# Performance work log

Measured on AMD Instinct MI355X. Metric: run time of the kernel, lower is better.

## Reference

```python
import jax, jax.numpy as jnp
import numpy as np

N, M = 32768, 12          # atoms, neighbors
ORIG, NBR, AF, HF = 92, 41, 64, 128
N_CONV = 3
ATOMS_PER = 32            # atoms per crystal
B = N // ATOMS_PER        # number of crystals
EPS = 1e-5                # BatchNorm eps


def softplus(x):
    return jnp.logaddexp(x, 0.0)


def setup_inputs() -> dict:
    key = jax.random.key(0)
    ks = jax.random.split(key, 24)
    s = 0.05
    return {
        "atom_fea": jax.random.normal(ks[0], (N, ORIG), jnp.float32),
        "nbr_fea": jax.random.normal(ks[1], (N, M, NBR), jnp.float32),
        "nbr_fea_idx": jax.random.randint(ks[2], (N, M), 0, N),
        "crystal_id": jnp.arange(N, dtype=jnp.int32) // ATOMS_PER,
        # embedding: Linear(ORIG -> AF)
        "emb_W": jax.random.normal(ks[3], (ORIG, AF), jnp.float32) * s,
        "emb_b": jnp.zeros((AF,), jnp.float32),
        # per-conv-layer params, stacked over N_CONV
        "conv_W": jax.random.normal(ks[4], (N_CONV, 2 * AF + NBR, 2 * AF), jnp.float32) * s,
        "conv_b": jnp.zeros((N_CONV, 2 * AF), jnp.float32),
        "bn1_g": jnp.ones((N_CONV, 2 * AF), jnp.float32),
        "bn1_b": jnp.zeros((N_CONV, 2 * AF), jnp.float32),
        "bn2_g": jnp.ones((N_CONV, AF), jnp.float32),
        "bn2_b": jnp.zeros((N_CONV, AF), jnp.float32),
        # head: conv_to_fc (AF->HF), fcs[0] (HF->HF), fc_out (HF->1)
        "fc1_W": jax.random.normal(ks[5], (AF, HF), jnp.float32) * s,
        "fc1_b": jnp.zeros((HF,), jnp.float32),
        "fc2_W": jax.random.normal(ks[6], (HF, HF), jnp.float32) * s,
        "fc2_b": jnp.zeros((HF,), jnp.float32),
        "out_W": jax.random.normal(ks[7], (HF, 1), jnp.float32) * s,
        "out_b": jnp.zeros((1,), jnp.float32),
    }


def _batchnorm(x, g, b):
    # training-mode BN over the batch (row) axis, biased variance like torch
    mu = x.mean(axis=0)
    var = x.var(axis=0)
    return (x - mu) * jax.lax.rsqrt(var + EPS) * g + b


def reference(atom_fea, nbr_fea, nbr_fea_idx, crystal_id,
              emb_W, emb_b, conv_W, conv_b, bn1_g, bn1_b, bn2_g, bn2_b,
              fc1_W, fc1_b, fc2_W, fc2_b, out_W, out_b):
    x = atom_fea @ emb_W + emb_b                              # (N, AF)
    for l in range(N_CONV):
        nbr_atom = x[nbr_fea_idx]                             # gather (N, M, AF)
        self_fea = jnp.broadcast_to(x[:, None, :], (N, M, AF))
        tot = jnp.concatenate([self_fea, nbr_atom, nbr_fea], axis=2)  # (N,M,2AF+NBR)
        g = tot @ conv_W[l] + conv_b[l]                       # (N, M, 2AF)
        g = _batchnorm(g.reshape(N * M, 2 * AF), bn1_g[l], bn1_b[l]).reshape(N, M, 2 * AF)
        nbr_filter = jax.nn.sigmoid(g[..., :AF])
        nbr_core = softplus(g[..., AF:])
        summed = jnp.sum(nbr_filter * nbr_core, axis=1)       # (N, AF)
        summed = _batchnorm(summed, bn2_g[l], bn2_b[l])
        x = softplus(x + summed)
    # mean pooling per crystal (equal-size crystals of ATOMS_PER atoms)
    pool = jax.ops.segment_sum(x, crystal_id, num_segments=B) / ATOMS_PER  # (B, AF)
    # seq2: softplus -> conv_to_fc -> dropout(p=0) -> softplus -> Linear -> softplus -> dropout(p=0)
    h = softplus(pool)
    h = softplus(h @ fc1_W + fc1_b)
    h = softplus(h @ fc2_W + fc2_b)
    return h @ out_W + out_b                                  # (B, 1)
```

## Files before the change

### kernel.cpp

```cpp
#include <hip/hip_runtime.h>
#include <cmath>

#define DEV __device__ __forceinline__

constexpr int NA    = 32768;
constexpr int M     = 12;
constexpr int ORIG  = 92;
constexpr int NBR   = 41;
constexpr int AF    = 64;
constexpr int C2    = 128;
constexpr int HF    = 128;
constexpr int NCONV = 3;
constexpr int NM    = NA * M;
constexpr int BB    = 1024;
constexpr int TA    = 4;
constexpr int RT    = TA * M;
constexpr int NTILES = NA / TA;
constexpr int GRID_CONV = 2048;
constexpr int GRID_APPLY = 2048;
constexpr int WLD   = 132;
constexpr int ALD   = 44;

DEV float fsig(float x) { return __builtin_amdgcn_rcpf(1.f + __expf(-x)); }
DEV float fsp (float x) { return fmaxf(x, 0.f) + __logf(1.f + __expf(-fabsf(x))); }

DEV void fma4(float4& a, float s, const float4 w) {
    a.x = fmaf(s, w.x, a.x); a.y = fmaf(s, w.y, a.y);
    a.z = fmaf(s, w.z, a.z); a.w = fmaf(s, w.w, a.w);
}
DEV void fma2(float2& a, float s, const float2 w) {
    a.x = fmaf(s, w.x, a.x); a.y = fmaf(s, w.y, a.y);
}
DEV float comp4(const float4 v, int i) { return i == 0 ? v.x : i == 1 ? v.y : i == 2 ? v.z : v.w; }
DEV void add2(float2& a, const float2 b) { a.x += b.x; a.y += b.y; }
DEV void sqa2(float2& a, const float2 b) { a.x = fmaf(b.x, b.x, a.x); a.y = fmaf(b.y, b.y, a.y); }
DEV float2 shxor2(const float2 v, int m) {
    float2 r; r.x = __shfl_xor(v.x, m, 64); r.y = __shfl_xor(v.y, m, 64); return r;
}
DEV unsigned bf16pair(float a, float b) {
    unsigned ua = __float_as_uint(a), ub = __float_as_uint(b);
    ua += 0x7fffu + ((ua >> 16) & 1u);
    ub += 0x7fffu + ((ub >> 16) & 1u);
    return (ua >> 16) | (ub & 0xffff0000u);
}
DEV float2 up2(unsigned u) {
    float2 r;
    r.x = __uint_as_float(u << 16);
    r.y = __uint_as_float(u & 0xffff0000u);
    return r;
}

template<bool FIRST>
__global__ __launch_bounds__(256, 4)
void spx_kernel(const float* __restrict__ xin,
                const float* __restrict__ summed,
                const float* __restrict__ ss2,
                const float* __restrict__ atom_fea,
                const float* __restrict__ embW,
                const float* __restrict__ embb,
                const float* __restrict__ W,
                const float* __restrict__ bias,
                float* __restrict__ xout,
                float* __restrict__ S,
                unsigned* __restrict__ Pb)
{
    __shared__ float xs[16][AF];
    __shared__ float af[FIRST ? 16 * ORIG : 4];

    const int a0 = blockIdx.x * 16, tid = threadIdx.x;

    if (FIRST) {
        for (int i = tid; i < 16 * ORIG; i += 256) af[i] = atom_fea[(size_t)a0 * ORIG + i];
        __syncthreads();
        const int row = tid >> 4, c4 = (tid & 15) * 4;
        float4 acc = *(const float4*)(embb + c4);
        #pragma unroll 4
        for (int k = 0; k < ORIG; ++k)
            fma4(acc, af[row * ORIG + k], *(const float4*)(embW + k * AF + c4));
        *(float4*)&xs[row][c4] = acc;
        *(float4*)(xout + (size_t)(a0 + row) * AF + c4) = acc;
    } else {
        const int row = tid >> 4, c4 = (tid & 15) * 4;
        const size_t o = (size_t)(a0 + row) * AF + c4;
        const float4 xi = *(const float4*)(xin + o);
        const float4 sm = *(const float4*)(summed + o);
        const float4 sc = *(const float4*)(ss2 + c4);
        const float4 sh = *(const float4*)(ss2 + AF + c4);
        float4 ov;
        ov.x = fsp(xi.x + fmaf(sm.x, sc.x, sh.x));
        ov.y = fsp(xi.y + fmaf(sm.y, sc.y, sh.y));
        ov.z = fsp(xi.z + fmaf(sm.z, sc.z, sh.z));
        ov.w = fsp(xi.w + fmaf(sm.w, sc.w, sh.w));
        *(float4*)&xs[row][c4] = ov;
        *(float4*)(xout + o) = ov;
    }
    __syncthreads();

    const int cid = tid & 31, rid = tid >> 5;
    const int c0 = cid * 8, r0 = rid * 2;
    const bool isS = (c0 < 128);
    const int cc = c0 & 127;
    const float* Wb = W + (isS ? 0 : AF * C2) + cc;
    float4 a00, a01, a10, a11;
    if (isS) { a00 = *(const float4*)(bias + cc); a01 = *(const float4*)(bias + cc + 4); }
    else     { a00 = {0,0,0,0}; a01 = {0,0,0,0}; }
    a10 = a00; a11 = a01;
    for (int k = 0; k < AF; ++k) {
        const float4 w0 = *(const float4*)(Wb + k * C2);
        const float4 w1 = *(const float4*)(Wb + k * C2 + 4);
        const float x0 = xs[r0][k], x1 = xs[r0 + 1][k];
        fma4(a00, x0, w0); fma4(a01, x0, w1);
        fma4(a10, x1, w0); fma4(a11, x1, w1);
    }
    if (isS) {
        *(float4*)(S + (size_t)(a0 + r0) * C2 + cc)     = a00;
        *(float4*)(S + (size_t)(a0 + r0) * C2 + cc + 4) = a01;
        *(float4*)(S + (size_t)(a0 + r0 + 1) * C2 + cc)     = a10;
        *(float4*)(S + (size_t)(a0 + r0 + 1) * C2 + cc + 4) = a11;
    } else {
        uint4 u0, u1;
        u0.x = bf16pair(a00.x, a00.y); u0.y = bf16pair(a00.z, a00.w);
        u0.z = bf16pair(a01.x, a01.y); u0.w = bf16pair(a01.z, a01.w);
        u1.x = bf16pair(a10.x, a10.y); u1.y = bf16pair(a10.z, a10.w);
        u1.z = bf16pair(a11.x, a11.y); u1.w = bf16pair(a11.z, a11.w);
        *(uint4*)(Pb + (size_t)(a0 + r0) * 64 + cc / 2)     = u0;
        *(uint4*)(Pb + (size_t)(a0 + r0 + 1) * 64 + cc / 2) = u1;
    }
}

__global__ __launch_bounds__(256, 4)
void conv8_kernel(const float* __restrict__ nbr_fea,
                  const int* __restrict__ idx,
                  const float* __restrict__ W2,
                  const float* __restrict__ S,
                  const unsigned* __restrict__ Pb,
                  float* __restrict__ P1s, float* __restrict__ P1q,
                  unsigned* __restrict__ gout)
{
    __shared__ float W2h[NBR * WLD];
    __shared__ float sA[RT * ALD];

    const int tid  = threadIdx.x;
    const int cid  = tid & 31;
    const int rid  = tid >> 5;
    const int c2   = cid * 2;
    const int r0   = rid * 6;
    const int atom = rid >> 1;

    const int q0 = blockIdx.x;

    int j[6];
    float2 svf, svc;
    float st[8];
    {
        const int n0 = q0 * TA;
        const int ib = n0 * M + r0;
        #pragma unroll
        for (int e = 0; e < 6; ++e) j[e] = idx[ib + e];
        svf = *(const float2*)(S + (size_t)(n0 + atom) * C2 + c2);
        svc = *(const float2*)(S + (size_t)(n0 + atom) * C2 + 64 + c2);
        const float* src = nbr_fea + (size_t)n0 * M * NBR;
        #pragma unroll
        for (int i = 0; i < 8; ++i)
            if (i < 7 || tid + 256 * i < RT * NBR) st[i] = src[tid + 256 * i];
    }

    for (int i = tid; i < NBR * 32; i += 256) {
        const int k = i >> 5, q = i & 31;
        *(float4*)&W2h[k * WLD + q * 4] = *(const float4*)(W2 + k * C2 + q * 4);
    }

    float2 sum_f = {0,0}, sum_c = {0,0}, sq_f = {0,0}, sq_c = {0,0};

    for (int it = 0; it < 4; ++it) {
        const int t  = q0 + it * GRID_CONV;
        const int n0 = t * TA;

        unsigned uf[6], uc[6];
        #pragma unroll
        for (int e = 0; e < 6; ++e) {
            uf[e] = Pb[(size_t)j[e] * 64 + cid];
            uc[e] = Pb[(size_t)j[e] * 64 + 32 + cid];
        }
        const float2 cf = svf, cc = svc;

        __syncthreads();
        #pragma unroll
        for (int i = 0; i < 8; ++i) {
            const int e = tid + 256 * i;
            if (i < 7 || e < RT * NBR) {
                const int r = (int)(((unsigned)e * 102301u) >> 22);
                sA[r * ALD + (e - r * NBR)] = st[i];
            }
        }
        __syncthreads();

        if (it < 3) {
            const int nn0 = (t + GRID_CONV) * TA;
            const int ib = nn0 * M + r0;
            #pragma unroll
            for (int e = 0; e < 6; ++e) j[e] = idx[ib + e];
            svf = *(const float2*)(S + (size_t)(nn0 + atom) * C2 + c2);
            svc = *(const float2*)(S + (size_t)(nn0 + atom) * C2 + 64 + c2);
            const float* src = nbr_fea + (size_t)nn0 * M * NBR;
            #pragma unroll
            for (int i = 0; i < 8; ++i)
                if (i < 7 || tid + 256 * i < RT * NBR) st[i] = src[tid + 256 * i];
        }

        float2 ef0 = {0,0}, ef1 = {0,0}, ef2 = {0,0}, ef3 = {0,0}, ef4 = {0,0}, ef5 = {0,0};
        float2 ec0 = {0,0}, ec1 = {0,0}, ec2 = {0,0}, ec3 = {0,0}, ec4 = {0,0}, ec5 = {0,0};
        const float* Ab = sA + r0 * ALD;
        #pragma unroll 2
        for (int k4 = 0; k4 < 10; ++k4) {
            const float4 a0 = *(const float4*)(Ab + 0 * ALD + k4 * 4);
            const float4 a1 = *(const float4*)(Ab + 1 * ALD + k4 * 4);
            const float4 a2 = *(const float4*)(Ab + 2 * ALD + k4 * 4);
            const float4 a3 = *(const float4*)(Ab + 3 * ALD + k4 * 4);
            const float4 a4 = *(const float4*)(Ab + 4 * ALD + k4 * 4);
            const float4 a5 = *(const float4*)(Ab + 5 * ALD + k4 * 4);
            #pragma unroll
            for (int kk = 0; kk < 4; ++kk) {
                const int k = 4 * k4 + kk;
                const float2 wf = *(const float2*)(W2h + k * WLD + c2);
                const float2 wc = *(const float2*)(W2h + k * WLD + 64 + c2);
                fma2(ef0, comp4(a0, kk), wf); fma2(ec0, comp4(a0, kk), wc);
                fma2(ef1, comp4(a1, kk), wf); fma2(ec1, comp4(a1, kk), wc);
                fma2(ef2, comp4(a2, kk), wf); fma2(ec2, comp4(a2, kk), wc);
                fma2(ef3, comp4(a3, kk), wf); fma2(ec3, comp4(a3, kk), wc);
                fma2(ef4, comp4(a4, kk), wf); fma2(ec4, comp4(a4, kk), wc);
                fma2(ef5, comp4(a5, kk), wf); fma2(ec5, comp4(a5, kk), wc);
            }
        }
        {
            const float2 wf = *(const float2*)(W2h + 40 * WLD + c2);
            const float2 wc = *(const float2*)(W2h + 40 * WLD + 64 + c2);
            const float b0 = Ab[0 * ALD + 40], b1 = Ab[1 * ALD + 40], b2 = Ab[2 * ALD + 40];
            const float b3 = Ab[3 * ALD + 40], b4 = Ab[4 * ALD + 40], b5 = Ab[5 * ALD + 40];
            fma2(ef0, b0, wf); fma2(ec0, b0, wc);
            fma2(ef1, b1, wf); fma2(ec1, b1, wc);
            fma2(ef2, b2, wf); fma2(ec2, b2, wc);
            fma2(ef3, b3, wf); fma2(ec3, b3, wc);
            fma2(ef4, b4, wf); fma2(ec4, b4, wc);
            fma2(ef5, b5, wf); fma2(ec5, b5, wc);
        }

        const size_t row0 = (size_t)(n0 * M + r0) * 64 + cid;
        {
            add2(ef0, cf); add2(ef0, up2(uf[0])); add2(ec0, cc); add2(ec0, up2(uc[0]));
            add2(ef1, cf); add2(ef1, up2(uf[1])); add2(ec1, cc); add2(ec1, up2(uc[1]));
            add2(ef2, cf); add2(ef2, up2(uf[2])); add2(ec2, cc); add2(ec2, up2(uc[2]));
            add2(ef3, cf); add2(ef3, up2(uf[3])); add2(ec3, cc); add2(ec3, up2(uc[3]));
            add2(ef4, cf); add2(ef4, up2(uf[4])); add2(ec4, cc); add2(ec4, up2(uc[4]));
            add2(ef5, cf); add2(ef5, up2(uf[5])); add2(ec5, cc); add2(ec5, up2(uc[5]));
            gout[row0 + 0 * 64]      = bf16pair(ef0.x, ef0.y);
            gout[row0 + 0 * 64 + 32] = bf16pair(ec0.x, ec0.y);
            gout[row0 + 1 * 64]      = bf16pair(ef1.x, ef1.y);
            gout[row0 + 1 * 64 + 32] = bf16pair(ec1.x, ec1.y);
            gout[row0 + 2 * 64]      = bf16pair(ef2.x, ef2.y);
            gout[row0 + 2 * 64 + 32] = bf16pair(ec2.x, ec2.y);
            gout[row0 + 3 * 64]      = bf16pair(ef3.x, ef3.y);
            gout[row0 + 3 * 64 + 32] = bf16pair(ec3.x, ec3.y);
            gout[row0 + 4 * 64]      = bf16pair(ef4.x, ef4.y);
            gout[row0 + 4 * 64 + 32] = bf16pair(ec4.x, ec4.y);
            gout[row0 + 5 * 64]      = bf16pair(ef5.x, ef5.y);
            gout[row0 + 5 * 64 + 32] = bf16pair(ec5.x, ec5.y);
            add2(sum_f, ef0); add2(sum_f, ef1); add2(sum_f, ef2);
            add2(sum_f, ef3); add2(sum_f, ef4); add2(sum_f, ef5);
            add2(sum_c, ec0); add2(sum_c, ec1); add2(sum_c, ec2);
            add2(sum_c, ec3); add2(sum_c, ec4); add2(sum_c, ec5);
            sqa2(sq_f, ef0); sqa2(sq_f, ef1); sqa2(sq_f, ef2);
            sqa2(sq_f, ef3); sqa2(sq_f, ef4); sqa2(sq_f, ef5);
            sqa2(sq_c, ec0); sqa2(sq_c, ec1); sqa2(sq_c, ec2);
            sqa2(sq_c, ec3); sqa2(sq_c, ec4); sqa2(sq_c, ec5);
        }
    }

    { float2 t2 = shxor2(sum_f, 32); add2(sum_f, t2); }
    { float2 t2 = shxor2(sum_c, 32); add2(sum_c, t2); }
    { float2 t2 = shxor2(sq_f, 32);  add2(sq_f, t2);  }
    { float2 t2 = shxor2(sq_c, 32);  add2(sq_c, t2);  }
    __syncthreads();
    const int w = tid >> 6;
    if ((tid & 32) == 0) {
        *(float2*)&sA[w * 128 + c2]            = sum_f;
        *(float2*)&sA[w * 128 + 64 + c2]       = sum_c;
        *(float2*)&sA[512 + w * 128 + c2]      = sq_f;
        *(float2*)&sA[512 + w * 128 + 64 + c2] = sq_c;
    }
    __syncthreads();
    if (tid < 128) {
        P1s[(size_t)blockIdx.x * C2 + tid] = sA[tid] + sA[128 + tid] + sA[256 + tid] + sA[384 + tid];
        P1q[(size_t)blockIdx.x * C2 + tid] = sA[512 + tid] + sA[512 + 128 + tid]
                                           + sA[512 + 256 + tid] + sA[512 + 384 + tid];
    }
}

__global__ __launch_bounds__(256)
void apply_g_kernel(const unsigned* __restrict__ g,
                    const float* __restrict__ ss1,
                    float* __restrict__ summed,
                    float* __restrict__ P2s, float* __restrict__ P2q)
{
    const int tid = threadIdx.x;
    const int al  = tid >> 5;
    const int c2  = tid & 31;
    const int cA  = 2 * c2;
    const float2 scf = *(const float2*)(ss1 + cA);
    const float2 scc = *(const float2*)(ss1 + 64 + cA);
    const float2 shf = *(const float2*)(ss1 + C2 + cA);
    const float2 shc = *(const float2*)(ss1 + C2 + 64 + cA);
    float2 ts = {0.f, 0.f}, tq = {0.f, 0.f};

    for (int grp = blockIdx.x; grp < NA / 8; grp += gridDim.x) {
        const int a = grp * 8 + al;
        const unsigned* gr = g + (size_t)a * M * 64 + c2;
        float2 acc = {0.f, 0.f};
        #pragma unroll
        for (int m = 0; m < M; ++m) {
            const unsigned uf = gr[m * 64];
            const unsigned us = gr[m * 64 + 32];
            const float2 f = up2(uf);
            const float2 s = up2(us);
            acc.x = fmaf(fsig(fmaf(f.x, scf.x, shf.x)), fsp(fmaf(s.x, scc.x, shc.x)), acc.x);
            acc.y = fmaf(fsig(fmaf(f.y, scf.y, shf.y)), fsp(fmaf(s.y, scc.y, shc.y)), acc.y);
        }
        *(float2*)(summed + (size_t)a * AF + cA) = acc;
        ts.x += acc.x; ts.y += acc.y;
        tq.x = fmaf(acc.x, acc.x, tq.x); tq.y = fmaf(acc.y, acc.y, tq.y);
    }

    __shared__ float2 rs[8][32], rq[8][32];
    rs[al][c2] = ts; rq[al][c2] = tq;
    __syncthreads();
    if (tid < 32) {
        float2 s = rs[0][tid], q = rq[0][tid];
        #pragma unroll
        for (int a = 1; a < 8; ++a) {
            s.x += rs[a][tid].x; s.y += rs[a][tid].y;
            q.x += rq[a][tid].x; q.y += rq[a][tid].y;
        }
        *(float2*)(P2s + (size_t)blockIdx.x * AF + 2 * tid) = s;
        *(float2*)(P2q + (size_t)blockIdx.x * AF + 2 * tid) = q;
    }
}

__global__ __launch_bounds__(256)
void bn_finalize_plain(const float* __restrict__ Ps, const float* __restrict__ Pq,
                       int npart, int C, float invn,
                       const float* __restrict__ gamma, const float* __restrict__ beta,
                       float* __restrict__ ss)
{
    __shared__ float sd[256];
    const int c = blockIdx.x, tid = threadIdx.x;
    float s = 0.f;
    for (int j = tid; j < npart; j += 256) s += Ps[(size_t)j * C + c];
    sd[tid] = s; __syncthreads();
    for (int st = 128; st > 0; st >>= 1) { if (tid < st) sd[tid] += sd[tid + st]; __syncthreads(); }
    const float total = sd[0];
    __syncthreads();
    float q = 0.f;
    for (int j = tid; j < npart; j += 256) q += Pq[(size_t)j * C + c];
    sd[tid] = q; __syncthreads();
    for (int st = 128; st > 0; st >>= 1) { if (tid < st) sd[tid] += sd[tid + st]; __syncthreads(); }
    if (tid == 0) {
        const float mean = total * invn;
        const float var  = sd[0] * invn - mean * mean;
        const float scl  = gamma[c] * rsqrtf(var + 1e-5f);
        ss[c]     = scl;
        ss[C + c] = beta[c] - mean * scl;
    }
}

__global__ __launch_bounds__(128)
void head_kernel(const float* __restrict__ x,
                 const float* __restrict__ summed,
                 const float* __restrict__ ss2,
                 const float* __restrict__ fc1W, const float* __restrict__ fc1b,
                 const float* __restrict__ fc2W, const float* __restrict__ fc2b,
                 const float* __restrict__ outW, const float* __restrict__ outb,
                 float* __restrict__ out)
{
    __shared__ float l0[AF], l1[HF], rr[2], hs[2][AF];
    const int b = blockIdx.x, tid = threadIdx.x;
    const int col = tid & 63, half = tid >> 6;
    {
        const float sc = ss2[col], sh = ss2[AF + col];
        float s = 0.f;
        #pragma unroll 4
        for (int a = half * 16; a < half * 16 + 16; ++a) {
            const size_t o = (size_t)(b * 32 + a) * AF + col;
            s += fsp(x[o] + fmaf(summed[o], sc, sh));
        }
        hs[half][col] = s;
    }
    __syncthreads();
    if (tid < AF) l0[tid] = fsp((hs[0][tid] + hs[1][tid]) * (1.f / 32.f));
    __syncthreads();
    float acc = fc1b[tid];
    #pragma unroll 4
    for (int k = 0; k < AF; ++k) acc = fmaf(l0[k], fc1W[k * HF + tid], acc);
    l1[tid] = fsp(acc);
    __syncthreads();
    acc = fc2b[tid];
    #pragma unroll 4
    for (int k = 0; k < HF; ++k) acc = fmaf(l1[k], fc2W[k * HF + tid], acc);
    float v = fsp(acc) * outW[tid];
    #pragma unroll
    for (int off = 32; off > 0; off >>= 1) v += __shfl_down(v, off, 64);
    if ((tid & 63) == 0) rr[tid >> 6] = v;
    __syncthreads();
    if (tid == 0) out[b] = rr[0] + rr[1] + outb[0];
}

extern "C" void kernel_launch(void* const* d_in, const int* in_sizes, int n_in,
                              void* d_out, int out_size, void* d_ws, size_t ws_size,
                              hipStream_t stream)
{
    const float* atom_fea = (const float*)d_in[0];
    const float* nbr_fea  = (const float*)d_in[1];
    const int*   nbr_idx  = (const int*)d_in[2];
    const float* emb_W  = (const float*)d_in[4];
    const float* emb_b  = (const float*)d_in[5];
    const float* conv_W = (const float*)d_in[6];
    const float* conv_b = (const float*)d_in[7];
    const float* bn1_g  = (const float*)d_in[8];
    const float* bn1_b  = (const float*)d_in[9];
    const float* bn2_g  = (const float*)d_in[10];
    const float* bn2_b  = (const float*)d_in[11];
    const float* fc1W   = (const float*)d_in[12];
    const float* fc1b   = (const float*)d_in[13];
    const float* fc2W   = (const float*)d_in[14];
    const float* fc2b   = (const float*)d_in[15];
    const float* outW   = (const float*)d_in[16];
    const float* outb   = (const float*)d_in[17];
    float* out = (float*)d_out;
    float* ws  = (float*)d_ws;

    float*    x_a    = ws;
    float*    x_b    = x_a + (size_t)NA * AF;
    float*    Sbuf   = x_b + (size_t)NA * AF;
    unsigned* Pb     = (unsigned*)(Sbuf + (size_t)NA * C2);
    float*    summed = (float*)(Pb + (size_t)NA * 64);
    float*    P1s    = summed + (size_t)NA * AF;
    float*    P1q    = P1s + (size_t)GRID_CONV * C2;
    float*    P2s    = P1q + (size_t)GRID_CONV * C2;
    float*    P2q    = P2s + (size_t)GRID_APPLY * AF;
    float*    ss1    = P2q + (size_t)GRID_APPLY * AF;
    float*    ss2    = ss1 + 2 * C2;
    unsigned* gbuf   = (unsigned*)(ss2 + 2 * AF);

    float* xcur = x_a;
    spx_kernel<true><<<NA / 16, 256, 0, stream>>>(nullptr, nullptr, nullptr,
                                                  atom_fea, emb_W, emb_b,
                                                  conv_W, conv_b, xcur, Sbuf, Pb);
    for (int l = 0; l < NCONV; ++l) {
        const float* W2 = conv_W + (size_t)l * (C2 + NBR) * C2 + (size_t)C2 * C2;
        conv8_kernel<<<GRID_CONV, 256, 0, stream>>>(nbr_fea, nbr_idx, W2,
                                                    Sbuf, Pb, P1s, P1q, gbuf);
        bn_finalize_plain<<<C2, 256, 0, stream>>>(P1s, P1q, GRID_CONV, C2, 1.f / (float)NM,
                                                  bn1_g + l * C2, bn1_b + l * C2, ss1);
        apply_g_kernel<<<GRID_APPLY, 256, 0, stream>>>(gbuf, ss1, summed, P2s, P2q);
        bn_finalize_plain<<<AF, 256, 0, stream>>>(P2s, P2q, GRID_APPLY, AF, 1.f / (float)NA,
                                                  bn2_g + l * AF, bn2_b + l * AF, ss2);
        if (l < NCONV - 1) {
            float* xnext = (xcur == x_a) ? x_b : x_a;
            spx_kernel<false><<<NA / 16, 256, 0, stream>>>(xcur, summed, ss2,
                                                           nullptr, nullptr, nullptr,
                                                           conv_W + (size_t)(l + 1) * (C2 + NBR) * C2,
                                                           conv_b + (size_t)(l + 1) * C2,
                                                           xnext, Sbuf, Pb);
            xcur = xnext;
        }
    }
    head_kernel<<<BB, 128, 0, stream>>>(xcur, summed, ss2,
                                        fc1W, fc1b, fc2W, fc2b, outW, outb, out);
}
```

Before: 646.9 us.

## Fuse BatchNorm finalize into conv and apply kernels via last-block atomic reduction

```diff
diff --git a/kernel.cpp b/kernel.cpp
--- a/kernel.cpp
+++ b/kernel.cpp
@@ -16,7 +16,7 @@
 constexpr int TA    = 4;
 constexpr int RT    = TA * M;
 constexpr int NTILES = NA / TA;
-constexpr int GRID_CONV = 2048;
+constexpr int GRID_CONV = 1024;
 constexpr int GRID_APPLY = 2048;
 constexpr int WLD   = 132;
 constexpr int ALD   = 44;
@@ -135,10 +135,15 @@
                   const float* __restrict__ S,
                   const unsigned* __restrict__ Pb,
                   float* __restrict__ P1s, float* __restrict__ P1q,
-                  unsigned* __restrict__ gout)
+                  unsigned* __restrict__ gout,
+                  unsigned* __restrict__ ctr,
+                  const float* __restrict__ gamma,
+                  const float* __restrict__ beta,
+                  float* __restrict__ ss, float invn)
 {
     __shared__ float W2h[NBR * WLD];
     __shared__ float sA[RT * ALD];
+    __shared__ int wflag;
 
     const int tid  = threadIdx.x;
     const int cid  = tid & 31;
@@ -172,17 +177,9 @@
 
     float2 sum_f = {0,0}, sum_c = {0,0}, sq_f = {0,0}, sq_c = {0,0};
 
-    for (int it = 0; it < 4; ++it) {
+    for (int it = 0; it < 8; ++it) {
         const int t  = q0 + it * GRID_CONV;
         const int n0 = t * TA;
-
-        unsigned uf[6], uc[6];
-        #pragma unroll
-        for (int e = 0; e < 6; ++e) {
-            uf[e] = Pb[(size_t)j[e] * 64 + cid];
-            uc[e] = Pb[(size_t)j[e] * 64 + 32 + cid];
-        }
-        const float2 cf = svf, cc = svc;
 
         __syncthreads();
         #pragma unroll
@@ -195,7 +192,15 @@
         }
         __syncthreads();
 
-        if (it < 3) {
+        unsigned uf[6], uc[6];
+        #pragma unroll
+        for (int e = 0; e < 6; ++e) {
+            uf[e] = Pb[(size_t)j[e] * 64 + cid];
+            uc[e] = Pb[(size_t)j[e] * 64 + 32 + cid];
+        }
+        const float2 cf = svf, cc = svc;
+
+        if (it < 7) {
             const int nn0 = (t + GRID_CONV) * TA;
             const int ib = nn0 * M + r0;
             #pragma unroll
@@ -290,9 +295,40 @@
     }
     __syncthreads();
     if (tid < 128) {
-        P1s[(size_t)blockIdx.x * C2 + tid] = sA[tid] + sA[128 + tid] + sA[256 + tid] + sA[384 + tid];
-        P1q[(size_t)blockIdx.x * C2 + tid] = sA[512 + tid] + sA[512 + 128 + tid]
-                                           + sA[512 + 256 + tid] + sA[512 + 384 + tid];
+        const float s = sA[tid] + sA[128 + tid] + sA[256 + tid] + sA[384 + tid];
+        const float q = sA[512 + tid] + sA[640 + tid] + sA[768 + tid] + sA[896 + tid];
+        P1s[(size_t)tid * GRID_CONV + blockIdx.x] = s;
+        P1q[(size_t)tid * GRID_CONV + blockIdx.x] = q;
+    }
+
+    __threadfence();
+    __syncthreads();
+    if (tid == 0) {
+        const unsigned old = atomicAdd(ctr, 1u);
+        wflag = (old == (unsigned)(gridDim.x - 1)) ? 1 : 0;
+    }
+    __syncthreads();
+    if (wflag) {
+        __threadfence();
+        const int c = tid & 127;
+        const float* Pcol = (tid < 128 ? P1s : P1q) + (size_t)c * GRID_CONV;
+        float s = 0.f;
+        #pragma unroll 4
+        for (int j4 = 0; j4 < GRID_CONV / 4; ++j4) {
+            const float4 v = *(const float4*)(Pcol + j4 * 4);
+            s += v.x + v.y + v.z + v.w;
+        }
+        sA[tid] = s;
+        __syncthreads();
+        if (tid < 128) {
+            const float mean = sA[tid] * invn;
+            const float var  = sA[128 + tid] * invn - mean * mean;
+            const float scl  = gamma[tid] * rsqrtf(var + 1e-5f);
+            ss[tid]      = scl;
+            ss[C2 + tid] = beta[tid] - mean * scl;
+        }
+        __syncthreads();
+        if (tid == 0) atomicExch(ctr, 0u);
     }
 }
 
@@ -300,8 +336,16 @@
 void apply_g_kernel(const unsigned* __restrict__ g,
                     const float* __restrict__ ss1,
                     float* __restrict__ summed,
-                    float* __restrict__ P2s, float* __restrict__ P2q)
+                    float* __restrict__ P2s, float* __restrict__ P2q,
+                    unsigned* __restrict__ ctr,
+                    const float* __restrict__ gamma,
+                    const float* __restrict__ beta,
+                    float* __restrict__ ss2out, float invn)
 {
+    __shared__ float2 rs[8][32], rq[8][32];
+    __shared__ float fin[128];
+    __shared__ int wflag;
+
     const int tid = threadIdx.x;
     const int al  = tid >> 5;
     const int c2  = tid & 31;
@@ -330,45 +374,49 @@
         tq.x = fmaf(acc.x, acc.x, tq.x); tq.y = fmaf(acc.y, acc.y, tq.y);
     }
 
-    __shared__ float2 rs[8][32], rq[8][32];
     rs[al][c2] = ts; rq[al][c2] = tq;
     __syncthreads();
-    if (tid < 32) {
-        float2 s = rs[0][tid], q = rq[0][tid];
+    if (tid < 128) {
+        const int c = tid & 63, isq = tid >> 6;
+        float s = 0.f;
         #pragma unroll
-        for (int a = 1; a < 8; ++a) {
-            s.x += rs[a][tid].x; s.y += rs[a][tid].y;
-            q.x += rq[a][tid].x; q.y += rq[a][tid].y;
-        }
-        *(float2*)(P2s + (size_t)blockIdx.x * AF + 2 * tid) = s;
-        *(float2*)(P2q + (size_t)blockIdx.x * AF + 2 * tid) = q;
-    }
-}
-
-__global__ __launch_bounds__(256)
-void bn_finalize_plain(const float* __restrict__ Ps, const float* __restrict__ Pq,
-                       int npart, int C, float invn,
-                       const float* __restrict__ gamma, const float* __restrict__ beta,
-                       float* __restrict__ ss)
-{
-    __shared__ float sd[256];
-    const int c = blockIdx.x, tid = threadIdx.x;
-    float s = 0.f;
-    for (int j = tid; j < npart; j += 256) s += Ps[(size_t)j * C + c];
-    sd[tid] = s; __syncthreads();
-    for (int st = 128; st > 0; st >>= 1) { if (tid < st) sd[tid] += sd[tid + st]; __syncthreads(); }
-    const float total = sd[0];
-    __syncthreads();
-    float q = 0.f;
-    for (int j = tid; j < npart; j += 256) q += Pq[(size_t)j * C + c];
-    sd[tid] = q; __syncthreads();
-    for (int st = 128; st > 0; st >>= 1) { if (tid < st) sd[tid] += sd[tid + st]; __syncthreads(); }
+        for (int a = 0; a < 8; ++a) {
+            const float2 v = isq ? rq[a][c >> 1] : rs[a][c >> 1];
+            s += (c & 1) ? v.y : v.x;
+        }
+        (isq ? P2q : P2s)[(size_t)c * GRID_APPLY + blockIdx.x] = s;
+    }
+
+    __threadfence();
+    __syncthreads();
     if (tid == 0) {
-        const float mean = total * invn;
-        const float var  = sd[0] * invn - mean * mean;
-        const float scl  = gamma[c] * rsqrtf(var + 1e-5f);
-        ss[c]     = scl;
-        ss[C + c] = beta[c] - mean * scl;
+        const unsigned old = atomicAdd(ctr, 1u);
+        wflag = (old == (unsigned)(gridDim.x - 1)) ? 1 : 0;
+    }
+    __syncthreads();
+    if (wflag) {
+        __threadfence();
+        if (tid < 128) {
+            const int c = tid & 63;
+            const float* Pcol = (tid < 64 ? P2s : P2q) + (size_t)c * GRID_APPLY;
+            float s = 0.f;
+            #pragma unroll 4
+            for (int j4 = 0; j4 < GRID_APPLY / 4; ++j4) {
+                const float4 v = *(const float4*)(Pcol + j4 * 4);
+                s += v.x + v.y + v.z + v.w;
+            }
+            fin[tid] = s;
+        }
+        __syncthreads();
+        if (tid < 64) {
+            const float mean = fin[tid] * invn;
+            const float var  = fin[64 + tid] * invn - mean * mean;
+            const float scl  = gamma[tid] * rsqrtf(var + 1e-5f);
+            ss2out[tid]      = scl;
+            ss2out[AF + tid] = beta[tid] - mean * scl;
+        }
+        __syncthreads();
+        if (tid == 0) atomicExch(ctr, 0u);
     }
 }
 
@@ -443,12 +491,15 @@
     unsigned* Pb     = (unsigned*)(Sbuf + (size_t)NA * C2);
     float*    summed = (float*)(Pb + (size_t)NA * 64);
     float*    P1s    = summed + (size_t)NA * AF;
-    float*    P1q    = P1s + (size_t)GRID_CONV * C2;
-    float*    P2s    = P1q + (size_t)GRID_CONV * C2;
-    float*    P2q    = P2s + (size_t)GRID_APPLY * AF;
-    float*    ss1    = P2q + (size_t)GRID_APPLY * AF;
+    float*    P1q    = P1s + (size_t)C2 * GRID_CONV;
+    float*    P2s    = P1q + (size_t)C2 * GRID_CONV;
+    float*    P2q    = P2s + (size_t)AF * GRID_APPLY;
+    float*    ss1    = P2q + (size_t)AF * GRID_APPLY;
     float*    ss2    = ss1 + 2 * C2;
-    unsigned* gbuf   = (unsigned*)(ss2 + 2 * AF);
+    unsigned* ctrs   = (unsigned*)(ss2 + 2 * AF);
+    unsigned* gbuf   = (unsigned*)(ctrs + 16);
+
+    hipMemsetAsync(ctrs, 0, 2 * sizeof(unsigned), stream);
 
     float* xcur = x_a;
     spx_kernel<true><<<NA / 16, 256, 0, stream>>>(nullptr, nullptr, nullptr,
@@ -457,12 +508,12 @@
     for (int l = 0; l < NCONV; ++l) {
         const float* W2 = conv_W + (size_t)l * (C2 + NBR) * C2 + (size_t)C2 * C2;
         conv8_kernel<<<GRID_CONV, 256, 0, stream>>>(nbr_fea, nbr_idx, W2,
-                                                    Sbuf, Pb, P1s, P1q, gbuf);
-        bn_finalize_plain<<<C2, 256, 0, stream>>>(P1s, P1q, GRID_CONV, C2, 1.f / (float)NM,
-                                                  bn1_g + l * C2, bn1_b + l * C2, ss1);
-        apply_g_kernel<<<GRID_APPLY, 256, 0, stream>>>(gbuf, ss1, summed, P2s, P2q);
-        bn_finalize_plain<<<AF, 256, 0, stream>>>(P2s, P2q, GRID_APPLY, AF, 1.f / (float)NA,
-                                                  bn2_g + l * AF, bn2_b + l * AF, ss2);
+                                                    Sbuf, Pb, P1s, P1q, gbuf,
+                                                    ctrs, bn1_g + l * C2, bn1_b + l * C2,
+                                                    ss1, 1.f / (float)NM);
+        apply_g_kernel<<<GRID_APPLY, 256, 0, stream>>>(gbuf, ss1, summed, P2s, P2q,
+                                                       ctrs + 1, bn2_g + l * AF, bn2_b + l * AF,
+                                                       ss2, 1.f / (float)NA);
         if (l < NCONV - 1) {
             float* xnext = (xcur == x_a) ? x_b : x_a;
             spx_kernel<false><<<NA / 16, 256, 0, stream>>>(xcur, summed, ss2,
```

Result: slower. 1.940 ms (+199.8%).
